# Kernel tuning notes

Hardware: AMD Instinct MI355X
Metric: run time of the kernel (lower is better)

Reference implementation:

```python
import jax, jax.numpy as jnp
import numpy as np

N = 50000   # nodes
E = 500000  # edges
F = 256     # node feature dim
ED = 64     # edge feature dim
H = 128     # hidden channels
O = 32      # out channels
NEG_SLOPE = 0.2
EPS = 1e-16


def setup_inputs() -> dict:
    key = jax.random.key(0)
    ks = jax.random.split(key, 16)
    s = 0.05
    return {
        "x": jax.random.normal(ks[0], (N, F), jnp.float32),
        "edge_index": jax.random.randint(ks[1], (2, E), 0, N, dtype=jnp.int32),
        "edge_attr": jax.random.normal(ks[2], (E, ED), jnp.float32),
        # layer 1 (embed): F -> H
        "W1": jax.random.normal(ks[3], (F, H), jnp.float32) * s,
        "att_src1": jax.random.normal(ks[4], (H,), jnp.float32) * s,
        "att_dst1": jax.random.normal(ks[5], (H,), jnp.float32) * s,
        "We1": jax.random.normal(ks[6], (ED, H), jnp.float32) * s,
        "att_edge1": jax.random.normal(ks[7], (H,), jnp.float32) * s,
        "b1": jnp.zeros((H,), jnp.float32),
        # layer 2 (classifier): H -> O
        "W2": jax.random.normal(ks[8], (H, O), jnp.float32) * s,
        "att_src2": jax.random.normal(ks[9], (O,), jnp.float32) * s,
        "att_dst2": jax.random.normal(ks[10], (O,), jnp.float32) * s,
        "We2": jax.random.normal(ks[11], (ED, O), jnp.float32) * s,
        "att_edge2": jax.random.normal(ks[12], (O,), jnp.float32) * s,
        "b2": jnp.zeros((O,), jnp.float32),
    }


def _add_self_loops_mean(src, dst, ea, n):
    # PyG add_self_loops(fill_value='mean'): self-loop edge_attr = mean of
    # incoming edge_attr per target node (0 for isolated nodes).
    ones = jnp.ones((ea.shape[0],), ea.dtype)
    cnt = jax.ops.segment_sum(ones, dst, num_segments=n)
    summ = jax.ops.segment_sum(ea, dst, num_segments=n)  # [n, ED]
    mean = summ / jnp.maximum(cnt, 1.0)[:, None]
    loop = jnp.arange(n, dtype=src.dtype)
    return (jnp.concatenate([src, loop]),
            jnp.concatenate([dst, loop]),
            jnp.concatenate([ea, mean], axis=0))


def _gat_conv(x, src, dst, ea, W, a_src, a_dst, We, a_edge, b):
    n = x.shape[0]
    src, dst, ea = _add_self_loops_mean(src, dst, ea, n)
    h = x @ W                       # [n, C]
    he = ea @ We                    # [E', C]
    a_s = h @ a_src                 # [n]
    a_d = h @ a_dst                 # [n]
    a_e = he @ a_edge               # [E']
    alpha = a_s[src] + a_d[dst] + a_e
    alpha = jax.nn.leaky_relu(alpha, NEG_SLOPE)
    # segment softmax over incoming edges of each target node
    m = jax.ops.segment_max(alpha, dst, num_segments=n)
    ex = jnp.exp(alpha - m[dst])
    denom = jax.ops.segment_sum(ex, dst, num_segments=n)
    coef = ex / (denom[dst] + EPS)
    out = jax.ops.segment_sum(coef[:, None] * h[src], dst, num_segments=n)
    return out + b


def reference(x, edge_index, edge_attr,
              W1, att_src1, att_dst1, We1, att_edge1, b1,
              W2, att_src2, att_dst2, We2, att_edge2, b2):
    src, dst = edge_index[0], edge_index[1]
    x1 = _gat_conv(x, src, dst, edge_attr, W1, att_src1, att_dst1, We1, att_edge1, b1)
    h = jax.nn.relu(x1)  # Dropout(0.5) is identity in eval mode
    out = _gat_conv(h, src, dst, edge_attr, W2, att_src2, att_dst2, We2, att_edge2, b2)
    return (out, h)
```

## Files before the change

kernel.cpp:

```cpp
#include <hip/hip_runtime.h>

#define N_NODES 50000
#define N_EDGES 500000
#define F_DIM 256
#define ED_DIM 64
#define H_DIM 128
#define O_DIM 32
#define NEG_SLOPE 0.2f
#define EPS_F 1e-16f
#define NEG_INF -3.4e38f

typedef __attribute__((ext_vector_type(8))) short short8;
typedef __attribute__((ext_vector_type(4))) float floatx4;

__device__ __forceinline__ unsigned short f2bf(float f) {
    union { float f; unsigned u; } c; c.f = f;
    unsigned u = c.u;
    return (unsigned short)((u + 0x7fffu + ((u >> 16) & 1u)) >> 16);
}
__device__ __forceinline__ float leaky(float a) { return a > 0.f ? a : a * NEG_SLOPE; }

__global__ void k_wevec(const float* __restrict__ We1, const float* __restrict__ aev1,
                        const float* __restrict__ We2, const float* __restrict__ aev2,
                        float* __restrict__ wv1, float* __restrict__ wv2) {
    int t = threadIdx.x;
    if (t < 64) {
        float s = 0.f;
        for (int c = 0; c < H_DIM; c++) s += We1[t * H_DIM + c] * aev1[c];
        wv1[t] = s;
    } else {
        int k = t - 64;
        float s = 0.f;
        for (int c = 0; c < O_DIM; c++) s += We2[k * O_DIM + c] * aev2[c];
        wv2[k] = s;
    }
}

__global__ void k_wconv(const float* __restrict__ W1, const float* __restrict__ W2,
                        unsigned short* __restrict__ W1T, unsigned short* __restrict__ W2T) {
    int gid = blockIdx.x * blockDim.x + threadIdx.x;
    int stride = gridDim.x * blockDim.x;
    for (int i = gid; i < H_DIM * F_DIM; i += stride) {
        int n = i >> 8, k = i & 255;
        W1T[i] = f2bf(W1[k * H_DIM + n]);
    }
    for (int i = gid; i < O_DIM * H_DIM; i += stride) {
        int n = i >> 7, k = i & 127;
        W2T[i] = f2bf(W2[k * O_DIM + n]);
    }
}

__global__ __launch_bounds__(256) void k_edge_ae(const float* __restrict__ ea,
                          const int* __restrict__ dst,
                          const float* __restrict__ wv1, const float* __restrict__ wv2,
                          float* __restrict__ ae1, float* __restrict__ ae2,
                          int* __restrict__ cnt) {
    int tid = threadIdx.x;
    int wave = tid >> 6, lane = tid & 63;
    int sub = lane & 15;
    int eo = lane >> 4;
    float4 w1 = ((const float4*)wv1)[sub];
    float4 w2 = ((const float4*)wv2)[sub];
    int e0 = (blockIdx.x * 4 + wave) * 4 + eo;
    int stride = gridDim.x * 16;
    for (int e = e0; e < N_EDGES; e += stride) {
        float4 q = *(const float4*)(ea + (size_t)e * ED_DIM + sub * 4);
        float s1 = q.x * w1.x + q.y * w1.y + q.z * w1.z + q.w * w1.w;
        float s2 = q.x * w2.x + q.y * w2.y + q.z * w2.z + q.w * w2.w;
#pragma unroll
        for (int o = 1; o < 16; o <<= 1) {
            s1 += __shfl_xor(s1, o);
            s2 += __shfl_xor(s2, o);
        }
        if (sub == 0) {
            ae1[e] = s1; ae2[e] = s2;
            atomicAdd(&cnt[dst[e]], 1);
        }
    }
}

__global__ void k_scan1(const int* __restrict__ cnt, int* __restrict__ bsum, int n) {
    __shared__ int sh[256];
    int b = blockIdx.x, t = threadIdx.x;
    int base = b * 1024;
    int s = 0;
    for (int j = 0; j < 4; j++) {
        int idx = base + t * 4 + j;
        if (idx < n) s += cnt[idx];
    }
    sh[t] = s; __syncthreads();
    for (int o = 128; o > 0; o >>= 1) {
        if (t < o) sh[t] += sh[t + o];
        __syncthreads();
    }
    if (t == 0) bsum[b] = sh[0];
}

__global__ void k_scan2(const int* __restrict__ bsum, int* __restrict__ bpre,
                        int* __restrict__ offs, int nb, int n) {
    if (threadIdx.x == 0) {
        int run = 0;
        for (int b = 0; b < nb; b++) { bpre[b] = run; run += bsum[b]; }
        offs[n] = run;
    }
}

__global__ void k_scan3(const int* __restrict__ cnt, const int* __restrict__ bpre,
                        int* __restrict__ offs, int n) {
    __shared__ int sh[256];
    int b = blockIdx.x, t = threadIdx.x;
    int base = b * 1024;
    int v[4]; int s = 0;
    for (int j = 0; j < 4; j++) {
        int idx = base + t * 4 + j;
        v[j] = (idx < n) ? cnt[idx] : 0;
        s += v[j];
    }
    sh[t] = s; __syncthreads();
    for (int o = 1; o < 256; o <<= 1) {
        int x = (t >= o) ? sh[t - o] : 0;
        __syncthreads();
        sh[t] += x;
        __syncthreads();
    }
    int texcl = sh[t] - s + bpre[b];
    int run = 0;
    for (int j = 0; j < 4; j++) {
        int idx = base + t * 4 + j;
        if (idx < n) offs[idx] = texcl + run;
        run += v[j];
    }
}

__global__ void k_scatter(const int* __restrict__ src, const int* __restrict__ dst,
                          const float* __restrict__ ae1, const float* __restrict__ ae2,
                          int* __restrict__ cursor,
                          int* __restrict__ csr_src,
                          float* __restrict__ csr_ae1, float* __restrict__ csr_ae2) {
    int e = blockIdx.x * blockDim.x + threadIdx.x;
    if (e >= N_EDGES) return;
    int d = dst[e];
    int p = atomicAdd(&cursor[d], 1);
    csr_src[p] = src[e];
    csr_ae1[p] = ae1[e];
    csr_ae2[p] = ae2[e];
}

__global__ __launch_bounds__(256) void k_gemm1(const float* __restrict__ A,
        const unsigned short* __restrict__ BT,
        const float* __restrict__ asv, const float* __restrict__ adv,
        float* __restrict__ C, float* __restrict__ a_s, float* __restrict__ a_d, int M) {
    __shared__ unsigned short As[128 * 40];
    __shared__ unsigned short Bs[128 * 40];
    int tid = threadIdx.x;
    int wave = tid >> 6, lane = tid & 63;
    int q = lane >> 4, r = lane & 15;
    int bm0 = blockIdx.x * 128;
    floatx4 acc[2][8];
#pragma unroll
    for (int a = 0; a < 2; a++)
#pragma unroll
        for (int b = 0; b < 8; b++) acc[a][b] = (floatx4){0.f, 0.f, 0.f, 0.f};

    int rr = tid >> 3;
    int kc = tid & 7;
    for (int k0 = 0; k0 < 256; k0 += 32) {
#pragma unroll
        for (int i = 0; i < 4; i++) {
            int row = rr + 32 * i;
            int gr = bm0 + row;
            float4 v = make_float4(0.f, 0.f, 0.f, 0.f);
            if (gr < M) v = *(const float4*)(A + (size_t)gr * 256 + k0 + kc * 4);
            unsigned lo = (unsigned)f2bf(v.x) | ((unsigned)f2bf(v.y) << 16);
            unsigned hi = (unsigned)f2bf(v.z) | ((unsigned)f2bf(v.w) << 16);
            *(uint2*)&As[row * 40 + kc * 4] = make_uint2(lo, hi);
        }
#pragma unroll
        for (int i = 0; i < 2; i++) {
            int idx = tid + 256 * i;
            int n = idx >> 2, ck = idx & 3;
            *(uint4*)&Bs[n * 40 + ck * 8] = *(const uint4*)(BT + n * 256 + k0 + ck * 8);
        }
        __syncthreads();
        short8 af[2], bf[8];
#pragma unroll
        for (int rt = 0; rt < 2; rt++)
            af[rt] = *(const short8*)&As[(wave * 32 + rt * 16 + r) * 40 + q * 8];
#pragma unroll
        for (int nt = 0; nt < 8; nt++)
            bf[nt] = *(const short8*)&Bs[(nt * 16 + r) * 40 + q * 8];
#pragma unroll
        for (int rt = 0; rt < 2; rt++)
#pragma unroll
            for (int nt = 0; nt < 8; nt++)
                acc[rt][nt] = __builtin_amdgcn_mfma_f32_16x16x32_bf16(af[rt], bf[nt], acc[rt][nt], 0, 0, 0);
        __syncthreads();
    }
#pragma unroll
    for (int rt = 0; rt < 2; rt++) {
        int rowb = bm0 + wave * 32 + rt * 16 + q * 4;
        float ps[4] = {0.f, 0.f, 0.f, 0.f}, pd[4] = {0.f, 0.f, 0.f, 0.f};
#pragma unroll
        for (int nt = 0; nt < 8; nt++) {
            int col = nt * 16 + r;
            float av = asv[col], dv = adv[col];
#pragma unroll
            for (int reg = 0; reg < 4; reg++) {
                float v = acc[rt][nt][reg];
                if (rowb + reg < M) C[(size_t)(rowb + reg) * 128 + col] = v;
                ps[reg] += v * av;
                pd[reg] += v * dv;
            }
        }
#pragma unroll
        for (int reg = 0; reg < 4; reg++) {
#pragma unroll
            for (int off = 1; off < 16; off <<= 1) {
                ps[reg] += __shfl_xor(ps[reg], off);
                pd[reg] += __shfl_xor(pd[reg], off);
            }
        }
        if (r == 0) {
#pragma unroll
            for (int reg = 0; reg < 4; reg++) {
                if (rowb + reg < M) { a_s[rowb + reg] = ps[reg]; a_d[rowb + reg] = pd[reg]; }
            }
        }
    }
}

__global__ __launch_bounds__(256) void k_gemm2(const float* __restrict__ A,
        const unsigned short* __restrict__ BT,
        const float* __restrict__ asv, const float* __restrict__ adv,
        float* __restrict__ C, float* __restrict__ a_s, float* __restrict__ a_d, int M) {
    __shared__ unsigned short As[128 * 40];
    __shared__ unsigned short Bs[32 * 40];
    int tid = threadIdx.x;
    int wave = tid >> 6, lane = tid & 63;
    int q = lane >> 4, r = lane & 15;
    int bm0 = blockIdx.x * 128;
    floatx4 acc[2][2];
#pragma unroll
    for (int a = 0; a < 2; a++)
#pragma unroll
        for (int b = 0; b < 2; b++) acc[a][b] = (floatx4){0.f, 0.f, 0.f, 0.f};

    int rr = tid >> 3;
    int kc = tid & 7;
    for (int k0 = 0; k0 < 128; k0 += 32) {
#pragma unroll
        for (int i = 0; i < 4; i++) {
            int row = rr + 32 * i;
            int gr = bm0 + row;
            float4 v = make_float4(0.f, 0.f, 0.f, 0.f);
            if (gr < M) v = *(const float4*)(A + (size_t)gr * 128 + k0 + kc * 4);
            unsigned lo = (unsigned)f2bf(v.x) | ((unsigned)f2bf(v.y) << 16);
            unsigned hi = (unsigned)f2bf(v.z) | ((unsigned)f2bf(v.w) << 16);
            *(uint2*)&As[row * 40 + kc * 4] = make_uint2(lo, hi);
        }
        if (tid < 128) {
            int n = tid >> 2, ck = tid & 3;
            *(uint4*)&Bs[n * 40 + ck * 8] = *(const uint4*)(BT + n * 128 + k0 + ck * 8);
        }
        __syncthreads();
        short8 af[2], bf[2];
#pragma unroll
        for (int rt = 0; rt < 2; rt++)
            af[rt] = *(const short8*)&As[(wave * 32 + rt * 16 + r) * 40 + q * 8];
#pragma unroll
        for (int nt = 0; nt < 2; nt++)
            bf[nt] = *(const short8*)&Bs[(nt * 16 + r) * 40 + q * 8];
#pragma unroll
        for (int rt = 0; rt < 2; rt++)
#pragma unroll
            for (int nt = 0; nt < 2; nt++)
                acc[rt][nt] = __builtin_amdgcn_mfma_f32_16x16x32_bf16(af[rt], bf[nt], acc[rt][nt], 0, 0, 0);
        __syncthreads();
    }
#pragma unroll
    for (int rt = 0; rt < 2; rt++) {
        int rowb = bm0 + wave * 32 + rt * 16 + q * 4;
        float ps[4] = {0.f, 0.f, 0.f, 0.f}, pd[4] = {0.f, 0.f, 0.f, 0.f};
#pragma unroll
        for (int nt = 0; nt < 2; nt++) {
            int col = nt * 16 + r;
            float av = asv[col], dv = adv[col];
#pragma unroll
            for (int reg = 0; reg < 4; reg++) {
                float v = acc[rt][nt][reg];
                if (rowb + reg < M) C[(size_t)(rowb + reg) * 32 + col] = v;
                ps[reg] += v * av;
                pd[reg] += v * dv;
            }
        }
#pragma unroll
        for (int reg = 0; reg < 4; reg++) {
#pragma unroll
            for (int off = 1; off < 16; off <<= 1) {
                ps[reg] += __shfl_xor(ps[reg], off);
                pd[reg] += __shfl_xor(pd[reg], off);
            }
        }
        if (r == 0) {
#pragma unroll
            for (int reg = 0; reg < 4; reg++) {
                if (rowb + reg < M) { a_s[rowb + reg] = ps[reg]; a_d[rowb + reg] = pd[reg]; }
            }
        }
    }
}

template <bool RELU>
__global__ __launch_bounds__(256) void k_agg128(const float* __restrict__ h,
                         const float* __restrict__ a_s, const float* __restrict__ a_d,
                         const int* __restrict__ offs, const int* __restrict__ csr_src,
                         const float* __restrict__ csr_ae,
                         const float* __restrict__ bias,
                         float* __restrict__ out) {
    int wave = threadIdx.x >> 6, lane = threadIdx.x & 63;
    int i = blockIdx.x * 4 + wave;
    int r = lane & 15;
    int g = lane >> 4;
    int rs = offs[i], re = offs[i + 1];
    int deg = re - rs;
    float adl = a_d[i];
    float sum_ae = 0.f, amax = NEG_INF;
    for (int el = rs + lane; el < re; el += 64) {
        float aev = csr_ae[el];
        float a = leaky(a_s[csr_src[el]] + adl + aev);
        sum_ae += aev;
        amax = fmaxf(amax, a);
    }
#pragma unroll
    for (int o = 32; o > 0; o >>= 1) {
        sum_ae += __shfl_xor(sum_ae, o);
        amax = fmaxf(amax, __shfl_xor(amax, o));
    }
    float loop_ae = sum_ae / (float)(deg > 1 ? deg : 1);
    float al = leaky(a_s[i] + adl + loop_ae);
    float m = fmaxf(amax, al);
    float exs = __expf(al - m);
    float4 acc0 = {0.f, 0.f, 0.f, 0.f}, acc1 = {0.f, 0.f, 0.f, 0.f};
    float dsum = 0.f;
    for (int base = rs; base < re; base += 64) {
        int el = base + lane;
        float ex = 0.f; int s = 0;
        if (el < re) {
            s = csr_src[el];
            float a = leaky(a_s[s] + adl + csr_ae[el]);
            ex = __expf(a - m);
        }
        dsum += ex;
        int nv = (re - base) < 64 ? (re - base) : 64;
        int kmax = (nv + 3) >> 2;
        for (int k = 0; k < kmax; k++) {
            int t = g + 4 * k;
            float ext = __shfl(ex, t);
            int st = __shfl(s, t);
            if (t < nv) {
                const float4* hr = (const float4*)(h + (size_t)st * 128);
                float4 v0 = hr[r * 2], v1 = hr[r * 2 + 1];
                acc0.x += ext * v0.x; acc0.y += ext * v0.y; acc0.z += ext * v0.z; acc0.w += ext * v0.w;
                acc1.x += ext * v1.x; acc1.y += ext * v1.y; acc1.z += ext * v1.z; acc1.w += ext * v1.w;
            }
        }
    }
#pragma unroll
    for (int o = 32; o > 0; o >>= 1) dsum += __shfl_xor(dsum, o);
    float* a0 = (float*)&acc0; float* a1 = (float*)&acc1;
#pragma unroll
    for (int c = 0; c < 4; c++) {
        a0[c] += __shfl_xor(a0[c], 16); a0[c] += __shfl_xor(a0[c], 32);
        a1[c] += __shfl_xor(a1[c], 16); a1[c] += __shfl_xor(a1[c], 32);
    }
    if (g == 0) {
        float denom = dsum + exs;
        float inv = 1.0f / (denom + EPS_F);
        const float4* hr = (const float4*)(h + (size_t)i * 128);
        float4 h0 = hr[r * 2], h1 = hr[r * 2 + 1];
        const float4* bp = (const float4*)bias;
        float4 b0 = bp[r * 2], b1 = bp[r * 2 + 1];
        float4 o0, o1;
        o0.x = (a0[0] + exs * h0.x) * inv + b0.x;
        o0.y = (a0[1] + exs * h0.y) * inv + b0.y;
        o0.z = (a0[2] + exs * h0.z) * inv + b0.z;
        o0.w = (a0[3] + exs * h0.w) * inv + b0.w;
        o1.x = (a1[0] + exs * h1.x) * inv + b1.x;
        o1.y = (a1[1] + exs * h1.y) * inv + b1.y;
        o1.z = (a1[2] + exs * h1.z) * inv + b1.z;
        o1.w = (a1[3] + exs * h1.w) * inv + b1.w;
        if (RELU) {
            o0.x = fmaxf(o0.x, 0.f); o0.y = fmaxf(o0.y, 0.f); o0.z = fmaxf(o0.z, 0.f); o0.w = fmaxf(o0.w, 0.f);
            o1.x = fmaxf(o1.x, 0.f); o1.y = fmaxf(o1.y, 0.f); o1.z = fmaxf(o1.z, 0.f); o1.w = fmaxf(o1.w, 0.f);
        }
        float4* op = (float4*)(out + (size_t)i * 128);
        op[r * 2] = o0;
        op[r * 2 + 1] = o1;
    }
}

__global__ __launch_bounds__(256) void k_agg32(const float* __restrict__ h,
                        const float* __restrict__ a_s, const float* __restrict__ a_d,
                        const int* __restrict__ offs, const int* __restrict__ csr_src,
                        const float* __restrict__ csr_ae,
                        const float* __restrict__ bias,
                        float* __restrict__ out) {
    int wave = threadIdx.x >> 6, lane = threadIdx.x & 63;
    int i = blockIdx.x * 4 + wave;
    int r = lane & 15;
    int g = lane >> 4;
    int rs = offs[i], re = offs[i + 1];
    int deg = re - rs;
    float adl = a_d[i];
    float sum_ae = 0.f, amax = NEG_INF;
    for (int el = rs + lane; el < re; el += 64) {
        float aev = csr_ae[el];
        float a = leaky(a_s[csr_src[el]] + adl + aev);
        sum_ae += aev;
        amax = fmaxf(amax, a);
    }
#pragma unroll
    for (int o = 32; o > 0; o >>= 1) {
        sum_ae += __shfl_xor(sum_ae, o);
        amax = fmaxf(amax, __shfl_xor(amax, o));
    }
    float loop_ae = sum_ae / (float)(deg > 1 ? deg : 1);
    float al = leaky(a_s[i] + adl + loop_ae);
    float m = fmaxf(amax, al);
    float exs = __expf(al - m);
    float2 acc = {0.f, 0.f};
    float dsum = 0.f;
    for (int base = rs; base < re; base += 64) {
        int el = base + lane;
        float ex = 0.f; int s = 0;
        if (el < re) {
            s = csr_src[el];
            float a = leaky(a_s[s] + adl + csr_ae[el]);
            ex = __expf(a - m);
        }
        dsum += ex;
        int nv = (re - base) < 64 ? (re - base) : 64;
        int kmax = (nv + 3) >> 2;
        for (int k = 0; k < kmax; k++) {
            int t = g + 4 * k;
            float ext = __shfl(ex, t);
            int st = __shfl(s, t);
            if (t < nv) {
                float2 v = ((const float2*)(h + (size_t)st * 32))[r];
                acc.x += ext * v.x; acc.y += ext * v.y;
            }
        }
    }
#pragma unroll
    for (int o = 32; o > 0; o >>= 1) dsum += __shfl_xor(dsum, o);
    acc.x += __shfl_xor(acc.x, 16); acc.x += __shfl_xor(acc.x, 32);
    acc.y += __shfl_xor(acc.y, 16); acc.y += __shfl_xor(acc.y, 32);
    if (g == 0) {
        float denom = dsum + exs;
        float inv = 1.0f / (denom + EPS_F);
        float2 hv = ((const float2*)(h + (size_t)i * 32))[r];
        float2 bv = ((const float2*)bias)[r];
        float2 ov;
        ov.x = (acc.x + exs * hv.x) * inv + bv.x;
        ov.y = (acc.y + exs * hv.y) * inv + bv.y;
        ((float2*)(out + (size_t)i * 32))[r] = ov;
    }
}

extern "C" void kernel_launch(void* const* d_in, const int* in_sizes, int n_in,
                              void* d_out, int out_size, void* d_ws, size_t ws_size,
                              hipStream_t stream) {
    const float* x    = (const float*)d_in[0];
    const int* ei     = (const int*)d_in[1];
    const float* ea   = (const float*)d_in[2];
    const float* W1   = (const float*)d_in[3];
    const float* as1v = (const float*)d_in[4];
    const float* ad1v = (const float*)d_in[5];
    const float* We1  = (const float*)d_in[6];
    const float* aev1 = (const float*)d_in[7];
    const float* b1   = (const float*)d_in[8];
    const float* W2   = (const float*)d_in[9];
    const float* as2v = (const float*)d_in[10];
    const float* ad2v = (const float*)d_in[11];
    const float* We2  = (const float*)d_in[12];
    const float* aev2 = (const float*)d_in[13];
    const float* b2   = (const float*)d_in[14];

    const int* src = ei;
    const int* dst = ei + N_EDGES;

    char* w = (char*)d_ws;
    size_t off = 0;
    auto alloc = [&](size_t bytes) -> void* {
        void* p = w + off;
        off += bytes;
        off = (off + 255) & ~(size_t)255;
        return p;
    };
    float* h1      = (float*)alloc((size_t)N_NODES * H_DIM * 4);
    float* h2      = (float*)alloc((size_t)N_NODES * O_DIM * 4);
    float* ae1     = (float*)alloc((size_t)N_EDGES * 4);
    float* ae2     = (float*)alloc((size_t)N_EDGES * 4);
    int* cnt       = (int*)alloc((size_t)N_NODES * 4);
    int* offs      = (int*)alloc((size_t)(N_NODES + 1) * 4);
    int* cursor    = (int*)alloc((size_t)N_NODES * 4);
    int* csr_src   = (int*)alloc((size_t)N_EDGES * 4);
    float* csr_ae1 = (float*)alloc((size_t)N_EDGES * 4);
    float* csr_ae2 = (float*)alloc((size_t)N_EDGES * 4);
    int* bsum      = (int*)alloc(64 * 4);
    int* bpre      = (int*)alloc(64 * 4);
    float* wv1     = (float*)alloc(64 * 4);
    float* wv2     = (float*)alloc(64 * 4);
    float* a_s1    = (float*)alloc((size_t)N_NODES * 4);
    float* a_d1    = (float*)alloc((size_t)N_NODES * 4);
    float* a_s2    = (float*)alloc((size_t)N_NODES * 4);
    float* a_d2    = (float*)alloc((size_t)N_NODES * 4);
    unsigned short* W1T = (unsigned short*)alloc((size_t)H_DIM * F_DIM * 2);
    unsigned short* W2T = (unsigned short*)alloc((size_t)O_DIM * H_DIM * 2);

    hipMemsetAsync(cnt, 0, (size_t)N_NODES * 4, stream);

    k_wevec<<<1, 128, 0, stream>>>(We1, aev1, We2, aev2, wv1, wv2);
    k_wconv<<<32, 256, 0, stream>>>(W1, W2, W1T, W2T);
    k_edge_ae<<<4096, 256, 0, stream>>>(ea, dst, wv1, wv2, ae1, ae2, cnt);
    int nb = (N_NODES + 1023) / 1024;
    k_scan1<<<nb, 256, 0, stream>>>(cnt, bsum, N_NODES);
    k_scan2<<<1, 64, 0, stream>>>(bsum, bpre, offs, nb, N_NODES);
    k_scan3<<<nb, 256, 0, stream>>>(cnt, bpre, offs, N_NODES);
    hipMemcpyAsync(cursor, offs, (size_t)N_NODES * 4, hipMemcpyDeviceToDevice, stream);
    k_scatter<<<(N_EDGES + 255) / 256, 256, 0, stream>>>(src, dst, ae1, ae2, cursor,
                                                         csr_src, csr_ae1, csr_ae2);

    float* out = (float*)d_out;
    float* h_out = out + (size_t)N_NODES * O_DIM;

    k_gemm1<<<(N_NODES + 127) / 128, 256, 0, stream>>>(x, W1T, as1v, ad1v,
                                                       h1, a_s1, a_d1, N_NODES);
    k_agg128<true><<<(N_NODES + 3) / 4, 256, 0, stream>>>(h1, a_s1, a_d1, offs,
                                                          csr_src, csr_ae1, b1, h_out);

    k_gemm2<<<(N_NODES + 127) / 128, 256, 0, stream>>>(h_out, W2T, as2v, ad2v,
                                                       h2, a_s2, a_d2, N_NODES);
    k_agg32<<<(N_NODES + 3) / 4, 256, 0, stream>>>(h2, a_s2, a_d2, offs,
                                                   csr_src, csr_ae2, b2, out);
}
```

Baseline: 416.2 us.

## Fuse gemm1 with edge pass, pack CSR records, drop softmax max pass

Merges the weight-prep kernels into one launch and runs the layer-1 GEMM concurrently with the edge-attention/degree-count pass in a single fused grid. The scatter now writes a packed float4 CSR record (src, ae1, ae2, a_s1[src]), and scan3 initialises the cursor directly, removing a memcpy. The aggregation kernels drop the separate max-reduction pass and compute unnormalised exponentials in one sweep. k_agg32 is widened to float4 per lane. Skipping the max subtraction risks overflow if attention logits are large, and the packed CSR raises scatter write bytes.

```diff
diff --git a/kernel.cpp b/kernel.cpp
--- a/kernel.cpp
+++ b/kernel.cpp
@@ -8,7 +8,9 @@
 #define O_DIM 32
 #define NEG_SLOPE 0.2f
 #define EPS_F 1e-16f
-#define NEG_INF -3.4e38f
+
+#define GB1 391
+#define EDGE_BLOCKS 4096
 
 typedef __attribute__((ext_vector_type(8))) short short8;
 typedef __attribute__((ext_vector_type(4))) float floatx4;
@@ -20,26 +22,27 @@
 }
 __device__ __forceinline__ float leaky(float a) { return a > 0.f ? a : a * NEG_SLOPE; }
 
-__global__ void k_wevec(const float* __restrict__ We1, const float* __restrict__ aev1,
-                        const float* __restrict__ We2, const float* __restrict__ aev2,
-                        float* __restrict__ wv1, float* __restrict__ wv2) {
-    int t = threadIdx.x;
-    if (t < 64) {
-        float s = 0.f;
-        for (int c = 0; c < H_DIM; c++) s += We1[t * H_DIM + c] * aev1[c];
-        wv1[t] = s;
-    } else {
-        int k = t - 64;
-        float s = 0.f;
-        for (int c = 0; c < O_DIM; c++) s += We2[k * O_DIM + c] * aev2[c];
-        wv2[k] = s;
-    }
-}
-
-__global__ void k_wconv(const float* __restrict__ W1, const float* __restrict__ W2,
-                        unsigned short* __restrict__ W1T, unsigned short* __restrict__ W2T) {
-    int gid = blockIdx.x * blockDim.x + threadIdx.x;
-    int stride = gridDim.x * blockDim.x;
+__global__ void k_prep(const float* __restrict__ We1, const float* __restrict__ aev1,
+                       const float* __restrict__ We2, const float* __restrict__ aev2,
+                       float* __restrict__ wv1, float* __restrict__ wv2,
+                       const float* __restrict__ W1, const float* __restrict__ W2,
+                       unsigned short* __restrict__ W1T, unsigned short* __restrict__ W2T) {
+    if (blockIdx.x == 32) {
+        int t = threadIdx.x;
+        if (t < 64) {
+            float s = 0.f;
+            for (int c = 0; c < H_DIM; c++) s += We1[t * H_DIM + c] * aev1[c];
+            wv1[t] = s;
+        } else if (t < 128) {
+            int k = t - 64;
+            float s = 0.f;
+            for (int c = 0; c < O_DIM; c++) s += We2[k * O_DIM + c] * aev2[c];
+            wv2[k] = s;
+        }
+        return;
+    }
+    int gid = blockIdx.x * 256 + threadIdx.x;
+    const int stride = 32 * 256;
     for (int i = gid; i < H_DIM * F_DIM; i += stride) {
         int n = i >> 8, k = i & 255;
         W1T[i] = f2bf(W1[k * H_DIM + n]);
@@ -50,31 +53,113 @@
     }
 }
 
-__global__ __launch_bounds__(256) void k_edge_ae(const float* __restrict__ ea,
-                          const int* __restrict__ dst,
-                          const float* __restrict__ wv1, const float* __restrict__ wv2,
-                          float* __restrict__ ae1, float* __restrict__ ae2,
-                          int* __restrict__ cnt) {
+__global__ __launch_bounds__(256) void k_fused1(
+        const float* __restrict__ A, const unsigned short* __restrict__ BT,
+        const float* __restrict__ asv, const float* __restrict__ adv,
+        float* __restrict__ C, float* __restrict__ a_s, float* __restrict__ a_d,
+        const float* __restrict__ ea, const int* __restrict__ dst,
+        const float* __restrict__ wv1, const float* __restrict__ wv2,
+        float2* __restrict__ ae12, int* __restrict__ cnt) {
+    __shared__ unsigned short As[128 * 40];
+    __shared__ unsigned short Bs[128 * 40];
     int tid = threadIdx.x;
     int wave = tid >> 6, lane = tid & 63;
-    int sub = lane & 15;
-    int eo = lane >> 4;
-    float4 w1 = ((const float4*)wv1)[sub];
-    float4 w2 = ((const float4*)wv2)[sub];
-    int e0 = (blockIdx.x * 4 + wave) * 4 + eo;
-    int stride = gridDim.x * 16;
-    for (int e = e0; e < N_EDGES; e += stride) {
-        float4 q = *(const float4*)(ea + (size_t)e * ED_DIM + sub * 4);
-        float s1 = q.x * w1.x + q.y * w1.y + q.z * w1.z + q.w * w1.w;
-        float s2 = q.x * w2.x + q.y * w2.y + q.z * w2.z + q.w * w2.w;
-#pragma unroll
-        for (int o = 1; o < 16; o <<= 1) {
-            s1 += __shfl_xor(s1, o);
-            s2 += __shfl_xor(s2, o);
-        }
-        if (sub == 0) {
-            ae1[e] = s1; ae2[e] = s2;
-            atomicAdd(&cnt[dst[e]], 1);
+
+    if (blockIdx.x >= GB1) {
+        int bid = blockIdx.x - GB1;
+        int sub = lane & 15, eo = lane >> 4;
+        float4 w1 = ((const float4*)wv1)[sub];
+        float4 w2 = ((const float4*)wv2)[sub];
+        int e0 = (bid * 4 + wave) * 4 + eo;
+        const int stride = EDGE_BLOCKS * 16;
+        for (int e = e0; e < N_EDGES; e += stride) {
+            float4 q = *(const float4*)(ea + (size_t)e * ED_DIM + sub * 4);
+            float s1 = q.x * w1.x + q.y * w1.y + q.z * w1.z + q.w * w1.w;
+            float s2 = q.x * w2.x + q.y * w2.y + q.z * w2.z + q.w * w2.w;
+#pragma unroll
+            for (int o = 1; o < 16; o <<= 1) {
+                s1 += __shfl_xor(s1, o);
+                s2 += __shfl_xor(s2, o);
+            }
+            if (sub == 0) {
+                ae12[e] = make_float2(s1, s2);
+                atomicAdd(&cnt[dst[e]], 1);
+            }
+        }
+        return;
+    }
+
+    int q = lane >> 4, r = lane & 15;
+    int bm0 = blockIdx.x * 128;
+    floatx4 acc[2][8];
+#pragma unroll
+    for (int a = 0; a < 2; a++)
+#pragma unroll
+        for (int b = 0; b < 8; b++) acc[a][b] = (floatx4){0.f, 0.f, 0.f, 0.f};
+
+    int rr = tid >> 3;
+    int kc = tid & 7;
+    for (int k0 = 0; k0 < 256; k0 += 32) {
+#pragma unroll
+        for (int i = 0; i < 4; i++) {
+            int row = rr + 32 * i;
+            int gr = bm0 + row;
+            float4 v = make_float4(0.f, 0.f, 0.f, 0.f);
+            if (gr < N_NODES) v = *(const float4*)(A + (size_t)gr * 256 + k0 + kc * 4);
+            unsigned lo = (unsigned)f2bf(v.x) | ((unsigned)f2bf(v.y) << 16);
+            unsigned hi = (unsigned)f2bf(v.z) | ((unsigned)f2bf(v.w) << 16);
+            *(uint2*)&As[row * 40 + kc * 4] = make_uint2(lo, hi);
+        }
+#pragma unroll
+        for (int i = 0; i < 2; i++) {
+            int idx = tid + 256 * i;
+            int n = idx >> 2, ck = idx & 3;
+            *(uint4*)&Bs[n * 40 + ck * 8] = *(const uint4*)(BT + n * 256 + k0 + ck * 8);
+        }
+        __syncthreads();
+        short8 af[2], bf[8];
+#pragma unroll
+        for (int rt = 0; rt < 2; rt++)
+            af[rt] = *(const short8*)&As[(wave * 32 + rt * 16 + r) * 40 + q * 8];
+#pragma unroll
+        for (int nt = 0; nt < 8; nt++)
+            bf[nt] = *(const short8*)&Bs[(nt * 16 + r) * 40 + q * 8];
+#pragma unroll
+        for (int rt = 0; rt < 2; rt++)
+#pragma unroll
+            for (int nt = 0; nt < 8; nt++)
+                acc[rt][nt] = __builtin_amdgcn_mfma_f32_16x16x32_bf16(af[rt], bf[nt], acc[rt][nt], 0, 0, 0);
+        __syncthreads();
+    }
+#pragma unroll
+    for (int rt = 0; rt < 2; rt++) {
+        int rowb = bm0 + wave * 32 + rt * 16 + q * 4;
+        float ps[4] = {0.f, 0.f, 0.f, 0.f}, pd[4] = {0.f, 0.f, 0.f, 0.f};
+#pragma unroll
+        for (int nt = 0; nt < 8; nt++) {
+            int col = nt * 16 + r;
+            float av = asv[col], dv = adv[col];
+#pragma unroll
+            for (int reg = 0; reg < 4; reg++) {
+                float v = acc[rt][nt][reg];
+                if (rowb + reg < N_NODES) C[(size_t)(rowb + reg) * 128 + col] = v;
+                ps[reg] += v * av;
+                pd[reg] += v * dv;
+            }
+        }
+#pragma unroll
+        for (int reg = 0; reg < 4; reg++) {
+#pragma unroll
+            for (int off = 1; off < 16; off <<= 1) {
+                ps[reg] += __shfl_xor(ps[reg], off);
+                pd[reg] += __shfl_xor(pd[reg], off);
+            }
+        }
+        if (r == 0) {
+#pragma unroll
+            for (int reg = 0; reg < 4; reg++) {
+                if (rowb + reg < N_NODES) { a_s[rowb + reg] = ps[reg]; a_d[rowb + reg] = pd[reg]; }
+            }
         }
     }
 }
@@ -106,7 +191,7 @@
 }
 
 __global__ void k_scan3(const int* __restrict__ cnt, const int* __restrict__ bpre,
-                        int* __restrict__ offs, int n) {
+                        int* __restrict__ offs, int* __restrict__ cursor, int n) {
     __shared__ int sh[256];
     int b = blockIdx.x, t = threadIdx.x;
     int base = b * 1024;
@@ -127,194 +212,28 @@
     int run = 0;
     for (int j = 0; j < 4; j++) {
         int idx = base + t * 4 + j;
-        if (idx < n) offs[idx] = texcl + run;
+        if (idx < n) { offs[idx] = texcl + run; cursor[idx] = texcl + run; }
         run += v[j];
     }
 }
 
-__global__ void k_scatter(const int* __restrict__ src, const int* __restrict__ dst,
-                          const float* __restrict__ ae1, const float* __restrict__ ae2,
-                          int* __restrict__ cursor,
-                          int* __restrict__ csr_src,
-                          float* __restrict__ csr_ae1, float* __restrict__ csr_ae2) {
+__global__ __launch_bounds__(256) void k_scatter(const int* __restrict__ src, const int* __restrict__ dst,
+                          const float2* __restrict__ ae12, const float* __restrict__ a_s1,
+                          int* __restrict__ cursor, float4* __restrict__ csr) {
     int e = blockIdx.x * blockDim.x + threadIdx.x;
     if (e >= N_EDGES) return;
+    int s = src[e];
     int d = dst[e];
+    float2 a = ae12[e];
+    float as = a_s1[s];
     int p = atomicAdd(&cursor[d], 1);
-    csr_src[p] = src[e];
-    csr_ae1[p] = ae1[e];
-    csr_ae2[p] = ae2[e];
-}
-
-__global__ __launch_bounds__(256) void k_gemm1(const float* __restrict__ A,
-        const unsigned short* __restrict__ BT,
-        const float* __restrict__ asv, const float* __restrict__ adv,
-        float* __restrict__ C, float* __restrict__ a_s, float* __restrict__ a_d, int M) {
-    __shared__ unsigned short As[128 * 40];
-    __shared__ unsigned short Bs[128 * 40];
-    int tid = threadIdx.x;
-    int wave = tid >> 6, lane = tid & 63;
-    int q = lane >> 4, r = lane & 15;
-    int bm0 = blockIdx.x * 128;
-    floatx4 acc[2][8];
-#pragma unroll
-    for (int a = 0; a < 2; a++)
-#pragma unroll
-        for (int b = 0; b < 8; b++) acc[a][b] = (floatx4){0.f, 0.f, 0.f, 0.f};
-
-    int rr = tid >> 3;
-    int kc = tid & 7;
-    for (int k0 = 0; k0 < 256; k0 += 32) {
-#pragma unroll
-        for (int i = 0; i < 4; i++) {
-            int row = rr + 32 * i;
-            int gr = bm0 + row;
-            float4 v = make_float4(0.f, 0.f, 0.f, 0.f);
-            if (gr < M) v = *(const float4*)(A + (size_t)gr * 256 + k0 + kc * 4);
-            unsigned lo = (unsigned)f2bf(v.x) | ((unsigned)f2bf(v.y) << 16);
-            unsigned hi = (unsigned)f2bf(v.z) | ((unsigned)f2bf(v.w) << 16);
-            *(uint2*)&As[row * 40 + kc * 4] = make_uint2(lo, hi);
-        }
-#pragma unroll
-        for (int i = 0; i < 2; i++) {
-            int idx = tid + 256 * i;
-            int n = idx >> 2, ck = idx & 3;
-            *(uint4*)&Bs[n * 40 + ck * 8] = *(const uint4*)(BT + n * 256 + k0 + ck * 8);
-        }
-        __syncthreads();
-        short8 af[2], bf[8];
-#pragma unroll
-        for (int rt = 0; rt < 2; rt++)
-            af[rt] = *(const short8*)&As[(wave * 32 + rt * 16 + r) * 40 + q * 8];
-#pragma unroll
-        for (int nt = 0; nt < 8; nt++)
-            bf[nt] = *(const short8*)&Bs[(nt * 16 + r) * 40 + q * 8];
-#pragma unroll
-        for (int rt = 0; rt < 2; rt++)
-#pragma unroll
-            for (int nt = 0; nt < 8; nt++)
-                acc[rt][nt] = __builtin_amdgcn_mfma_f32_16x16x32_bf16(af[rt], bf[nt], acc[rt][nt], 0, 0, 0);
-        __syncthreads();
-    }
-#pragma unroll
-    for (int rt = 0; rt < 2; rt++) {
-        int rowb = bm0 + wave * 32 + rt * 16 + q * 4;
-        float ps[4] = {0.f, 0.f, 0.f, 0.f}, pd[4] = {0.f, 0.f, 0.f, 0.f};
-#pragma unroll
-        for (int nt = 0; nt < 8; nt++) {
-            int col = nt * 16 + r;
-            float av = asv[col], dv = adv[col];
-#pragma unroll
-            for (int reg = 0; reg < 4; reg++) {
-                float v = acc[rt][nt][reg];
-                if (rowb + reg < M) C[(size_t)(rowb + reg) * 128 + col] = v;
-                ps[reg] += v * av;
-                pd[reg] += v * dv;
-            }
-        }
-#pragma unroll
-        for (int reg = 0; reg < 4; reg++) {
-#pragma unroll
-            for (int off = 1; off < 16; off <<= 1) {
-                ps[reg] += __shfl_xor(ps[reg], off);
-                pd[reg] += __shfl_xor(pd[reg], off);
-            }
-        }
-        if (r == 0) {
-#pragma unroll
-            for (int reg = 0; reg < 4; reg++) {
-                if (rowb + reg < M) { a_s[rowb + reg] = ps[reg]; a_d[rowb + reg] = pd[reg]; }
-            }
-        }
-    }
-}
-
-__global__ __launch_bounds__(256) void k_gemm2(const float* __restrict__ A,
-        const unsigned short* __restrict__ BT,
-        const float* __restrict__ asv, const float* __restrict__ adv,
-        float* __restrict__ C, float* __restrict__ a_s, float* __restrict__ a_d, int M) {
-    __shared__ unsigned short As[128 * 40];
-    __shared__ unsigned short Bs[32 * 40];
-    int tid = threadIdx.x;
-    int wave = tid >> 6, lane = tid & 63;
-    int q = lane >> 4, r = lane & 15;
-    int bm0 = blockIdx.x * 128;
-    floatx4 acc[2][2];
-#pragma unroll
-    for (int a = 0; a < 2; a++)
-#pragma unroll
-        for (int b = 0; b < 2; b++) acc[a][b] = (floatx4){0.f, 0.f, 0.f, 0.f};
-
-    int rr = tid >> 3;
-    int kc = tid & 7;
-    for (int k0 = 0; k0 < 128; k0 += 32) {
-#pragma unroll
-        for (int i = 0; i < 4; i++) {
-            int row = rr + 32 * i;
-            int gr = bm0 + row;
-            float4 v = make_float4(0.f, 0.f, 0.f, 0.f);
-            if (gr < M) v = *(const float4*)(A + (size_t)gr * 128 + k0 + kc * 4);
-            unsigned lo = (unsigned)f2bf(v.x) | ((unsigned)f2bf(v.y) << 16);
-            unsigned hi = (unsigned)f2bf(v.z) | ((unsigned)f2bf(v.w) << 16);
-            *(uint2*)&As[row * 40 + kc * 4] = make_uint2(lo, hi);
-        }
-        if (tid < 128) {
-            int n = tid >> 2, ck = tid & 3;
-            *(uint4*)&Bs[n * 40 + ck * 8] = *(const uint4*)(BT + n * 128 + k0 + ck * 8);
-        }
-        __syncthreads();
-        short8 af[2], bf[2];
-#pragma unroll
-        for (int rt = 0; rt < 2; rt++)
-            af[rt] = *(const short8*)&As[(wave * 32 + rt * 16 + r) * 40 + q * 8];
-#pragma unroll
-        for (int nt = 0; nt < 2; nt++)
-            bf[nt] = *(const short8*)&Bs[(nt * 16 + r) * 40 + q * 8];
-#pragma unroll
-        for (int rt = 0; rt < 2; rt++)
-#pragma unroll
-            for (int nt = 0; nt < 2; nt++)
-                acc[rt][nt] = __builtin_amdgcn_mfma_f32_16x16x32_bf16(af[rt], bf[nt], acc[rt][nt], 0, 0, 0);
-        __syncthreads();
-    }
-#pragma unroll
-    for (int rt = 0; rt < 2; rt++) {
-        int rowb = bm0 + wave * 32 + rt * 16 + q * 4;
-        float ps[4] = {0.f, 0.f, 0.f, 0.f}, pd[4] = {0.f, 0.f, 0.f, 0.f};
-#pragma unroll
-        for (int nt = 0; nt < 2; nt++) {
-            int col = nt * 16 + r;
-            float av = asv[col], dv = adv[col];
-#pragma unroll
-            for (int reg = 0; reg < 4; reg++) {
-                float v = acc[rt][nt][reg];
-                if (rowb + reg < M) C[(size_t)(rowb + reg) * 32 + col] = v;
-                ps[reg] += v * av;
-                pd[reg] += v * dv;
-            }
-        }
-#pragma unroll
-        for (int reg = 0; reg < 4; reg++) {
-#pragma unroll
-            for (int off = 1; off < 16; off <<= 1) {
-                ps[reg] += __shfl_xor(ps[reg], off);
-                pd[reg] += __shfl_xor(pd[reg], off);
-            }
-        }
-        if (r == 0) {
-#pragma unroll
-            for (int reg = 0; reg < 4; reg++) {
-                if (rowb + reg < M) { a_s[rowb + reg] = ps[reg]; a_d[rowb + reg] = pd[reg]; }
-            }
-        }
-    }
+    csr[p] = make_float4(__int_as_float(s), a.x, a.y, as);
 }
 
 template <bool RELU>
 __global__ __launch_bounds__(256) void k_agg128(const float* __restrict__ h,
                          const float* __restrict__ a_s, const float* __restrict__ a_d,
-                         const int* __restrict__ offs, const int* __restrict__ csr_src,
-                         const float* __restrict__ csr_ae,
+                         const int* __restrict__ offs, const float4* __restrict__ csr,
                          const float* __restrict__ bias,
                          float* __restrict__ out) {
     int wave = threadIdx.x >> 6, lane = threadIdx.x & 63;
@@ -324,33 +243,18 @@
     int rs = offs[i], re = offs[i + 1];
     int deg = re - rs;
     float adl = a_d[i];
-    float sum_ae = 0.f, amax = NEG_INF;
-    for (int el = rs + lane; el < re; el += 64) {
-        float aev = csr_ae[el];
-        float a = leaky(a_s[csr_src[el]] + adl + aev);
-        sum_ae += aev;
-        amax = fmaxf(amax, a);
-    }
-#pragma unroll
-    for (int o = 32; o > 0; o >>= 1) {
-        sum_ae += __shfl_xor(sum_ae, o);
-        amax = fmaxf(amax, __shfl_xor(amax, o));
-    }
-    float loop_ae = sum_ae / (float)(deg > 1 ? deg : 1);
-    float al = leaky(a_s[i] + adl + loop_ae);
-    float m = fmaxf(amax, al);
-    float exs = __expf(al - m);
     float4 acc0 = {0.f, 0.f, 0.f, 0.f}, acc1 = {0.f, 0.f, 0.f, 0.f};
-    float dsum = 0.f;
+    float dsum = 0.f, sum_ae = 0.f;
     for (int base = rs; base < re; base += 64) {
         int el = base + lane;
-        float ex = 0.f; int s = 0;
+        float ex = 0.f, aev = 0.f; int s = 0;
         if (el < re) {
-            s = csr_src[el];
-            float a = leaky(a_s[s] + adl + csr_ae[el]);
-            ex = __expf(a - m);
-        }
-        dsum += ex;
+            float4 c = csr[el];
+            s = __float_as_int(c.x);
+            aev = c.y;
+            ex = __expf(leaky(c.w + adl + aev));
+        }
+        dsum += ex; sum_ae += aev;
         int nv = (re - base) < 64 ? (re - base) : 64;
         int kmax = (nv + 3) >> 2;
         for (int k = 0; k < kmax; k++) {
@@ -366,7 +270,13 @@
         }
     }
 #pragma unroll
-    for (int o = 32; o > 0; o >>= 1) dsum += __shfl_xor(dsum, o);
+    for (int o = 32; o > 0; o >>= 1) {
+        dsum += __shfl_xor(dsum, o);
+        sum_ae += __shfl_xor(sum_ae, o);
+    }
+    float loop_ae = sum_ae / (float)(deg > 1 ? deg : 1);
+    float al = leaky(a_s[i] + adl + loop_ae);
+    float exs = __expf(al);
     float* a0 = (float*)&acc0; float* a1 = (float*)&acc1;
 #pragma unroll
     for (int c = 0; c < 4; c++) {
@@ -374,8 +284,7 @@
         a1[c] += __shfl_xor(a1[c], 16); a1[c] += __shfl_xor(a1[c], 32);
     }
     if (g == 0) {
-        float denom = dsum + exs;
-        float inv = 1.0f / (denom + EPS_F);
+        float inv = 1.0f / (dsum + exs + EPS_F);
         const float4* hr = (const float4*)(h + (size_t)i * 128);
         float4 h0 = hr[r * 2], h1 = hr[r * 2 + 1];
         const float4* bp = (const float4*)bias;
@@ -399,71 +308,146 @@
     }
 }
 
+__global__ __launch_bounds__(256) void k_gemm2(const float* __restrict__ A,
+        const unsigned short* __restrict__ BT,
+        const float* __restrict__ asv, const float* __restrict__ adv,
+        float* __restrict__ C, float* __restrict__ a_s, float* __restrict__ a_d, int M) {
+    __shared__ unsigned short As[128 * 40];
+    __shared__ unsigned short Bs[32 * 40];
+    int tid = threadIdx.x;
+    int wave = tid >> 6, lane = tid & 63;
+    int q = lane >> 4, r = lane & 15;
+    int bm0 = blockIdx.x * 128;
+    floatx4 acc[2][2];
+#pragma unroll
+    for (int a = 0; a < 2; a++)
+#pragma unroll
+        for (int b = 0; b < 2; b++) acc[a][b] = (floatx4){0.f, 0.f, 0.f, 0.f};
+
+    int rr = tid >> 3;
+    int kc = tid & 7;
+    for (int k0 = 0; k0 < 128; k0 += 32) {
+#pragma unroll
+        for (int i = 0; i < 4; i++) {
+            int row = rr + 32 * i;
+            int gr = bm0 + row;
+            float4 v = make_float4(0.f, 0.f, 0.f, 0.f);
+            if (gr < M) v = *(const float4*)(A + (size_t)gr * 128 + k0 + kc * 4);
+            unsigned lo = (unsigned)f2bf(v.x) | ((unsigned)f2bf(v.y) << 16);
+            unsigned hi = (unsigned)f2bf(v.z) | ((unsigned)f2bf(v.w) << 16);
+            *(uint2*)&As[row * 40 + kc * 4] = make_uint2(lo, hi);
+        }
+        if (tid < 128) {
+            int n = tid >> 2, ck = tid & 3;
+            *(uint4*)&Bs[n * 40 + ck * 8] = *(const uint4*)(BT + n * 128 + k0 + ck * 8);
+        }
+        __syncthreads();
+        short8 af[2], bf[2];
+#pragma unroll
+        for (int rt = 0; rt < 2; rt++)
+            af[rt] = *(const short8*)&As[(wave * 32 + rt * 16 + r) * 40 + q * 8];
+#pragma unroll
+        for (int nt = 0; nt < 2; nt++)
+            bf[nt] = *(const short8*)&Bs[(nt * 16 + r) * 40 + q * 8];
+#pragma unroll
+        for (int rt = 0; rt < 2; rt++)
+#pragma unroll
+            for (int nt = 0; nt < 2; nt++)
+                acc[rt][nt] = __builtin_amdgcn_mfma_f32_16x16x32_bf16(af[rt], bf[nt], acc[rt][nt], 0, 0, 0);
+        __syncthreads();
+    }
+#pragma unroll
+    for (int rt = 0; rt < 2; rt++) {
+        int rowb = bm0 + wave * 32 + rt * 16 + q * 4;
+        float ps[4] = {0.f, 0.f, 0.f, 0.f}, pd[4] = {0.f, 0.f, 0.f, 0.f};
+#pragma unroll
+        for (int nt = 0; nt < 2; nt++) {
+            int col = nt * 16 + r;
+            float av = asv[col], dv = adv[col];
+#pragma unroll
+            for (int reg = 0; reg < 4; reg++) {
+                float v = acc[rt][nt][reg];
+                if (rowb + reg < M) C[(size_t)(rowb + reg) * 32 + col] = v;
+                ps[reg] += v * av;
+                pd[reg] += v * dv;
+            }
+        }
+#pragma unroll
+        for (int reg = 0; reg < 4; reg++) {
+#pragma unroll
+            for (int off = 1; off < 16; off <<= 1) {
+                ps[reg] += __shfl_xor(ps[reg], off);
+                pd[reg] += __shfl_xor(pd[reg], off);
+            }
+        }
+        if (r == 0) {
+#pragma unroll
+            for (int reg = 0; reg < 4; reg++) {
+                if (rowb + reg < M) { a_s[rowb + reg] = ps[reg]; a_d[rowb + reg] = pd[reg]; }
+            }
+        }
+    }
+}
+
 __global__ __launch_bounds__(256) void k_agg32(const float* __restrict__ h,
                         const float* __restrict__ a_s, const float* __restrict__ a_d,
-                        const int* __restrict__ offs, const int* __restrict__ csr_src,
-                        const float* __restrict__ csr_ae,
+                        const int* __restrict__ offs, const float4* __restrict__ csr,
                         const float* __restrict__ bias,
                         float* __restrict__ out) {
     int wave = threadIdx.x >> 6, lane = threadIdx.x & 63;
     int i = blockIdx.x * 4 + wave;
-    int r = lane & 15;
-    int g = lane >> 4;
+    int r = lane & 7;
+    int g = lane >> 3;
     int rs = offs[i], re = offs[i + 1];
     int deg = re - rs;
     float adl = a_d[i];
-    float sum_ae = 0.f, amax = NEG_INF;
-    for (int el = rs + lane; el < re; el += 64) {
-        float aev = csr_ae[el];
-        float a = leaky(a_s[csr_src[el]] + adl + aev);
-        sum_ae += aev;
-        amax = fmaxf(amax, a);
-    }
-#pragma unroll
-    for (int o = 32; o > 0; o >>= 1) {
-        sum_ae += __shfl_xor(sum_ae, o);
-        amax = fmaxf(amax, __shfl_xor(amax, o));
-    }
-    float loop_ae = sum_ae / (float)(deg > 1 ? deg : 1);
-    float al = leaky(a_s[i] + adl + loop_ae);
-    float m = fmaxf(amax, al);
-    float exs = __expf(al - m);
-    float2 acc = {0.f, 0.f};
-    float dsum = 0.f;
+    float4 acc = {0.f, 0.f, 0.f, 0.f};
+    float dsum = 0.f, sum_ae = 0.f;
     for (int base = rs; base < re; base += 64) {
         int el = base + lane;
-        float ex = 0.f; int s = 0;
+        float ex = 0.f, aev = 0.f; int s = 0;
         if (el < re) {
-            s = csr_src[el];
-            float a = leaky(a_s[s] + adl + csr_ae[el]);
-            ex = __expf(a - m);
-        }
-        dsum += ex;
+            float4 c = csr[el];
+            s = __float_as_int(c.x);
+            aev = c.z;
+            ex = __expf(leaky(a_s[s] + adl + aev));
+        }
+        dsum += ex; sum_ae += aev;
         int nv = (re - base) < 64 ? (re - base) : 64;
-        int kmax = (nv + 3) >> 2;
+        int kmax = (nv + 7) >> 3;
         for (int k = 0; k < kmax; k++) {
-            int t = g + 4 * k;
+            int t = g + 8 * k;
             float ext = __shfl(ex, t);
             int st = __shfl(s, t);
             if (t < nv) {
-                float2 v = ((const float2*)(h + (size_t)st * 32))[r];
-                acc.x += ext * v.x; acc.y += ext * v.y;
-            }
-        }
-    }
-#pragma unroll
-    for (int o = 32; o > 0; o >>= 1) dsum += __shfl_xor(dsum, o);
-    acc.x += __shfl_xor(acc.x, 16); acc.x += __shfl_xor(acc.x, 32);
-    acc.y += __shfl_xor(acc.y, 16); acc.y += __shfl_xor(acc.y, 32);
+                float4 v = ((const float4*)(h + (size_t)st * 32))[r];
+                acc.x += ext * v.x; acc.y += ext * v.y; acc.z += ext * v.z; acc.w += ext * v.w;
+            }
+        }
+    }
+#pragma unroll
+    for (int o = 32; o > 0; o >>= 1) {
+        dsum += __shfl_xor(dsum, o);
+        sum_ae += __shfl_xor(sum_ae, o);
+    }
+    float loop_ae = sum_ae / (float)(deg > 1 ? deg : 1);
+    float al = leaky(a_s[i] + adl + loop_ae);
+    float exs = __expf(al);
+#pragma unroll
+    for (int o = 8; o < 64; o <<= 1) {
+        acc.x += __shfl_xor(acc.x, o); acc.y += __shfl_xor(acc.y, o);
+        acc.z += __shfl_xor(acc.z, o); acc.w += __shfl_xor(acc.w, o);
+    }
     if (g == 0) {
-        float denom = dsum + exs;
-        float inv = 1.0f / (denom + EPS_F);
-        float2 hv = ((const float2*)(h + (size_t)i * 32))[r];
-        float2 bv = ((const float2*)bias)[r];
-        float2 ov;
+        float inv = 1.0f / (dsum + exs + EPS_F);
+        float4 hv = ((const float4*)(h + (size_t)i * 32))[r];
+        float4 bv = ((const float4*)bias)[r];
+        float4 ov;
         ov.x = (acc.x + exs * hv.x) * inv + bv.x;
         ov.y = (acc.y + exs * hv.y) * inv + bv.y;
-        ((float2*)(out + (size_t)i * 32))[r] = ov;
+        ov.z = (acc.z + exs * hv.z) * inv + bv.z;
+        ov.w = (acc.w + exs * hv.w) * inv + bv.w;
+        ((float4*)(out + (size_t)i * 32))[r] = ov;
     }
 }
 
@@ -499,14 +483,11 @@
     };
     float* h1      = (float*)alloc((size_t)N_NODES * H_DIM * 4);
     float* h2      = (float*)alloc((size_t)N_NODES * O_DIM * 4);
-    float* ae1     = (float*)alloc((size_t)N_EDGES * 4);
-    float* ae2     = (float*)alloc((size_t)N_EDGES * 4);
+    float2* ae12   = (float2*)alloc((size_t)N_EDGES * 8);
     int* cnt       = (int*)alloc((size_t)N_NODES * 4);
     int* offs      = (int*)alloc((size_t)(N_NODES + 1) * 4);
     int* cursor    = (int*)alloc((size_t)N_NODES * 4);
-    int* csr_src   = (int*)alloc((size_t)N_EDGES * 4);
-    float* csr_ae1 = (float*)alloc((size_t)N_EDGES * 4);
-    float* csr_ae2 = (float*)alloc((size_t)N_EDGES * 4);
+    float4* csr    = (float4*)alloc((size_t)N_EDGES * 16);
     int* bsum      = (int*)alloc(64 * 4);
     int* bpre      = (int*)alloc(64 * 4);
     float* wv1     = (float*)alloc(64 * 4);
@@ -520,27 +501,28 @@
 
     hipMemsetAsync(cnt, 0, (size_t)N_NODES * 4, stream);
 
-    k_wevec<<<1, 128, 0, stream>>>(We1, aev1, We2, aev2, wv1, wv2);
-    k_wconv<<<32, 256, 0, stream>>>(W1, W2, W1T, W2T);
-    k_edge_ae<<<4096, 256, 0, stream>>>(ea, dst, wv1, wv2, ae1, ae2, cnt);
+    k_prep<<<33, 256, 0, stream>>>(We1, aev1, We2, aev2, wv1, wv2, W1, W2, W1T, W2T);
+
+    k_fused1<<<GB1 + EDGE_BLOCKS, 256, 0, stream>>>(x, W1T, as1v, ad1v,
+                                                    h1, a_s1, a_d1,
+                                                    ea, dst, wv1, wv2, ae12, cnt);
+
     int nb = (N_NODES + 1023) / 1024;
     k_scan1<<<nb, 256, 0, stream>>>(cnt, bsum, N_NODES);
     k_scan2<<<1, 64, 0, stream>>>(bsum, bpre, offs, nb, N_NODES);
-    k_scan3<<<nb, 256, 0, stream>>>(cnt, bpre, offs, N_NODES);
-    hipMemcpyAsync(cursor, offs, (size_t)N_NODES * 4, hipMemcpyDeviceToDevice, stream);
-    k_scatter<<<(N_EDGES + 255) / 256, 256, 0, stream>>>(src, dst, ae1, ae2, cursor,
-                                                         csr_src, csr_ae1, csr_ae2);
+    k_scan3<<<nb, 256, 0, stream>>>(cnt, bpre, offs, cursor, N_NODES);
+
+    k_scatter<<<(N_EDGES + 255) / 256, 256, 0, stream>>>(src, dst, ae12, a_s1,
+                                                         cursor, csr);
 
     float* out = (float*)d_out;
     float* h_out = out + (size_t)N_NODES * O_DIM;
 
-    k_gemm1<<<(N_NODES + 127) / 128, 256, 0, stream>>>(x, W1T, as1v, ad1v,
-                                                       h1, a_s1, a_d1, N_NODES);
     k_agg128<true><<<(N_NODES + 3) / 4, 256, 0, stream>>>(h1, a_s1, a_d1, offs,
-                                                          csr_src, csr_ae1, b1, h_out);
+                                                          csr, b1, h_out);
 
     k_gemm2<<<(N_NODES + 127) / 128, 256, 0, stream>>>(h_out, W2T, as2v, ad2v,
                                                        h2, a_s2, a_d2, N_NODES);
     k_agg32<<<(N_NODES + 3) / 4, 256, 0, stream>>>(h2, a_s2, a_d2, offs,
-                                                   csr_src, csr_ae2, b2, out);
-}
+                                                   csr, b2, out);
+}
```

New measurement: 406.7 us. 1.02x faster.
